# Kernel tuning notes

Hardware: AMD Instinct MI355X
Metric: run time of the kernel (lower is better)

## Reference

```python
import jax, jax.numpy as jnp
import numpy as np

N = 100000      # nodes
E = 300000      # edges
D_IN = 32       # input feature dim
D_MEM = 256     # memory dim
D_HID = 256     # hidden dim
D_TIME = 32     # time encoding dim
HEADS = 4
C = D_HID // 4  # per-head channels (GATConv out_channels)
D_OUT = 2


def gru_cell(x, h, wih, whh, bih, bhh):
    # torch.nn.GRUCell semantics, gate order (r, z, n)
    gi = x @ wih.T + bih
    gh = h @ whh.T + bhh
    ir, iz, inn = jnp.split(gi, 3, axis=-1)
    hr, hz, hn = jnp.split(gh, 3, axis=-1)
    r = jax.nn.sigmoid(ir + hr)
    z = jax.nn.sigmoid(iz + hz)
    n = jnp.tanh(inn + r * hn)
    return (1.0 - z) * n + z * h


def gat_layer(h, src, dst, W, a_src, a_dst, bias):
    # PyG GATConv(concat=True), default add_self_loops=True, negative_slope=0.2
    n = h.shape[0]
    xh = (h @ W.T).reshape(n, HEADS, C)              # [N,H,C]
    al_s = (xh * a_src).sum(-1)                      # [N,H]
    al_d = (xh * a_dst).sum(-1)                      # [N,H]
    loop = jnp.arange(n, dtype=src.dtype)
    s = jnp.concatenate([src, loop])
    d = jnp.concatenate([dst, loop])
    e = jax.nn.leaky_relu(al_s[s] + al_d[d], 0.2)    # [E+N,H]
    emax = jax.ops.segment_max(e, d, num_segments=n)
    ee = jnp.exp(e - emax[d])
    denom = jax.ops.segment_sum(ee, d, num_segments=n)
    alpha = ee / denom[d]                            # softmax over incoming edges
    out = jax.ops.segment_sum(alpha[:, :, None] * xh[s], d, num_segments=n)
    return out.reshape(n, HEADS * C) + bias


def setup_inputs() -> dict:
    key = jax.random.key(0)
    ks = jax.random.split(key, 32)
    w = lambda k, sh: jax.random.normal(k, sh, jnp.float32) * 0.05
    d_msg_in = 2 * D_MEM + D_IN + D_TIME  # 576
    return {
        "x": jax.random.normal(ks[0], (N, D_IN), jnp.float32),
        "timestamps": jax.random.uniform(ks[1], (E,), jnp.float32),
        "node_memory": jnp.zeros((N, D_MEM), jnp.float32),
        "last_update_time": jnp.zeros((N,), jnp.float32),
        "msg_w1": w(ks[2], (D_HID, d_msg_in)), "msg_b1": w(ks[3], (D_HID,)),
        "msg_w2": w(ks[4], (D_MEM, D_HID)), "msg_b2": w(ks[5], (D_MEM,)),
        "time_w1": w(ks[6], (D_TIME, 1)), "time_b1": w(ks[7], (D_TIME,)),
        "time_w2": w(ks[8], (D_TIME, D_TIME)), "time_b2": w(ks[9], (D_TIME,)),
        "gru_wih": w(ks[10], (3 * D_MEM, D_MEM)), "gru_whh": w(ks[11], (3 * D_MEM, D_MEM)),
        "gru_bih": w(ks[12], (3 * D_MEM,)), "gru_bhh": w(ks[13], (3 * D_MEM,)),
        "gat1_w": w(ks[14], (HEADS * C, D_MEM)), "gat1_asrc": w(ks[15], (HEADS, C)),
        "gat1_adst": w(ks[16], (HEADS, C)), "gat1_b": w(ks[17], (HEADS * C,)),
        "gat2_w": w(ks[18], (HEADS * C, D_HID)), "gat2_asrc": w(ks[19], (HEADS, C)),
        "gat2_adst": w(ks[20], (HEADS, C)), "gat2_b": w(ks[21], (HEADS * C,)),
        "cls_w1": w(ks[22], (D_HID // 2, D_HID)), "cls_b1": w(ks[23], (D_HID // 2,)),
        "cls_w2": w(ks[24], (D_OUT, D_HID // 2)), "cls_b2": w(ks[25], (D_OUT,)),
        "edge_index": jax.random.randint(ks[26], (2, E), 0, N, jnp.int32),
        "batch": jnp.zeros((N,), jnp.int32),
    }


def reference(x, timestamps, node_memory, last_update_time,
              msg_w1, msg_b1, msg_w2, msg_b2,
              time_w1, time_b1, time_w2, time_b2,
              gru_wih, gru_whh, gru_bih, gru_bhh,
              gat1_w, gat1_asrc, gat1_adst, gat1_b,
              gat2_w, gat2_asrc, gat2_adst, gat2_b,
              cls_w1, cls_b1, cls_w2, cls_b2,
              edge_index, batch):
    src, dst = edge_index[0], edge_index[1]
    edge_attr = x[src]                               # torch path: edge_attr=None -> x[edge_index[0]]
    current_time = timestamps.max()
    # --- compute_messages ---
    dt = (current_time - jnp.maximum(last_update_time[src], last_update_time[dst]))[:, None]
    te = jax.nn.relu(dt @ time_w1.T + time_b1) @ time_w2.T + time_b2
    mi = jnp.concatenate([node_memory[src], node_memory[dst], edge_attr, te], axis=-1)  # [E,576]
    msgs = jax.nn.relu(mi @ msg_w1.T + msg_b1) @ msg_w2.T + msg_b2                      # [E,256]
    # --- update_memory: fused segment-mean + batched GRU ---
    counts = jax.ops.segment_sum(jnp.ones((E,), msgs.dtype), dst, num_segments=N)
    agg = jax.ops.segment_sum(msgs, dst, num_segments=N) / jnp.maximum(counts, 1.0)[:, None]
    mem_new = gru_cell(agg, node_memory, gru_wih, gru_whh, gru_bih, gru_bhh)
    mem = jnp.where((counts > 0)[:, None], mem_new, node_memory)
    # --- GAT embedding layers (dropout inactive in eval) ---
    h = jax.nn.elu(gat_layer(mem, src, dst, gat1_w, gat1_asrc, gat1_adst, gat1_b))
    h = jax.nn.elu(gat_layer(h, src, dst, gat2_w, gat2_asrc, gat2_adst, gat2_b))
    # --- global mean pool (single graph, batch==0) + classifier ---
    gsum = jax.ops.segment_sum(h, batch, num_segments=1)
    gcnt = jax.ops.segment_sum(jnp.ones((N,), h.dtype), batch, num_segments=1)
    g = gsum / gcnt[:, None]
    logits = jax.nn.relu(g @ cls_w1.T + cls_b1) @ cls_w2.T + cls_b2
    return logits
```

## Files before the change

kernel.cpp:

```cpp
#include <hip/hip_runtime.h>

#define NN 100000
#define NE 300000
#define GPLANE 528

typedef float f32x4 __attribute__((ext_vector_type(4)));
typedef __bf16 bf16x8 __attribute__((ext_vector_type(8)));
typedef unsigned short ushort8v __attribute__((ext_vector_type(8)));

__device__ __forceinline__ int enc_f(float f) {
    int i = __float_as_int(f);
    return i >= 0 ? i : (i ^ 0x7fffffff);
}
__device__ __forceinline__ float dec_f(int i) {
    return __int_as_float(i >= 0 ? i : (i ^ 0x7fffffff));
}
__device__ __forceinline__ unsigned short f2bf(float f) {
    unsigned u = __float_as_uint(f);
    u += 0x7fffu + ((u >> 16) & 1u);
    return (unsigned short)(u >> 16);
}
__device__ __forceinline__ float bf2f(unsigned short u) {
    return __uint_as_float((unsigned)u << 16);
}

__global__ void k_dbg(float* out, float v) { out[0] = v; out[1] = v; }

__global__ void k_fill_i32(int* p, int v, int n) {
    int i = blockIdx.x * 256 + threadIdx.x;
    if (i < n) p[i] = v;
}

__global__ void k_pack_w_sub(const float* __restrict__ src, unsigned short* __restrict__ dst,
                             int OUT, int K, int stride, int off) {
    int i = blockIdx.x * 256 + threadIdx.x;
    if (i >= OUT * K) return;
    int o = i / K, k = i % K;
    int ob = o >> 6, n = (o >> 4) & 3, fr = o & 15;
    int step = k >> 5, kq = (k >> 3) & 3, j = k & 7;
    size_t dsti = ((((size_t)step * (OUT >> 6) + ob) * 4 + n) * 64 + (kq * 16 + fr)) * 8 + j;
    dst[dsti] = f2bf(src[(size_t)o * stride + off + k]);
}

__global__ void k_fold_te(const float* __restrict__ msg_w1, const float* __restrict__ tw2,
                          const float* __restrict__ tb2, const float* __restrict__ b1,
                          float* __restrict__ Mtd, float* __restrict__ b1eff) {
    int i = blockIdx.x * 256 + threadIdx.x;
    if (i < 256 * 32) {
        int o = i >> 5, col = i & 31;
        float s = 0.f;
        const float* w1d = msg_w1 + (size_t)o * 576 + 544;
#pragma unroll
        for (int c = 0; c < 32; ++c) s += w1d[c] * tw2[c * 32 + col];
        Mtd[i] = s;
        if (col == 0) {
            float sb = b1[o];
#pragma unroll
            for (int c = 0; c < 32; ++c) sb += w1d[c] * tb2[c];
            b1eff[o] = sb;
        }
    }
}

__global__ void k_timemax(const float* __restrict__ ts, int n, int* out) {
    float m = -INFINITY;
    int stride = gridDim.x * blockDim.x;
    for (int i = blockIdx.x * blockDim.x + threadIdx.x; i < n; i += stride)
        m = fmaxf(m, ts[i]);
    atomicMax(out, enc_f(m));
}

__global__ void k_counts(const int* __restrict__ ei, float* __restrict__ counts) {
    int stride = gridDim.x * blockDim.x;
    for (int i = blockIdx.x * blockDim.x + threadIdx.x; i < NE; i += stride)
        atomicAdd(&counts[ei[NE + i]], 1.f);
}

__global__ void k_scan1(const float* __restrict__ counts, int* __restrict__ rowptr,
                        int* __restrict__ bsum) {
    __shared__ int sh[256];
    int t = threadIdx.x;
    int i = blockIdx.x * 256 + t;
    int v = (i < NN) ? ((int)counts[i] + 1) : 0;
    sh[t] = v;
    __syncthreads();
    for (int off = 1; off < 256; off <<= 1) {
        int x = (t >= off) ? sh[t - off] : 0;
        __syncthreads();
        sh[t] += x;
        __syncthreads();
    }
    if (i < NN) rowptr[i + 1] = sh[t];
    if (t == 255) bsum[blockIdx.x] = sh[255];
}

__global__ void k_scan2(int* __restrict__ bsum, int nb) {
    __shared__ int sh[512];
    int t = threadIdx.x;
    sh[t] = (t < nb) ? bsum[t] : 0;
    __syncthreads();
    for (int off = 1; off < 512; off <<= 1) {
        int x = (t >= off) ? sh[t - off] : 0;
        __syncthreads();
        sh[t] += x;
        __syncthreads();
    }
    if (t < nb) bsum[t] = sh[t];
}

__global__ void k_scan3(int* __restrict__ rowptr, const int* __restrict__ bsum) {
    int i = blockIdx.x * 256 + threadIdx.x;
    if (i == 0) rowptr[0] = 0;
    if (i < NN) {
        int b = i >> 8;
        int off = b > 0 ? bsum[b - 1] : 0;
        rowptr[i + 1] += off;
    }
}

__global__ void k_copy_fill(const int* __restrict__ rowptr, int* __restrict__ fill) {
    int i = blockIdx.x * 256 + threadIdx.x;
    if (i < NN) fill[i] = rowptr[i];
}

__global__ void k_csr_fill(const int* __restrict__ ei, int* __restrict__ fill,
                           int* __restrict__ colidx) {
    int i = blockIdx.x * 256 + threadIdx.x;
    if (i < NE) {
        int d = ei[NE + i];
        int pos = atomicAdd(&fill[d], 1);
        colidx[pos] = ei[i];
    } else if (i < NE + NN) {
        int n = i - NE;
        int pos = atomicAdd(&fill[n], 1);
        colidx[pos] = n;
    }
}

__global__ void k_rowptrE(const int* __restrict__ rowptr, int* __restrict__ fillE) {
    int i = blockIdx.x * 256 + threadIdx.x;
    if (i < NN) fillE[i] = rowptr[i] - i;
}

__global__ void k_ecsr_fill(const int* __restrict__ ei, int* __restrict__ fillE,
                            int* __restrict__ esrc, int* __restrict__ edst) {
    int i = blockIdx.x * 256 + threadIdx.x;
    if (i < NE) {
        int d = ei[NE + i];
        int pos = atomicAdd(&fillE[d], 1);
        esrc[pos] = ei[i];
        edst[pos] = d;
    }
}

__global__ __launch_bounds__(512, 4) void k_pre1(
    const float* __restrict__ mem, const float* __restrict__ x,
    const unsigned short* __restrict__ w1ap, const unsigned short* __restrict__ w1bp,
    const unsigned short* __restrict__ w1cp,
    unsigned short* __restrict__ P13, unsigned short* __restrict__ P2,
    unsigned short* __restrict__ membf) {
    __shared__ unsigned short Af[2 * 8 * GPLANE];
    __shared__ unsigned short Axf[2 * 512];
    const int t = threadIdx.x;
    const int lane = t & 63, w = t >> 6;
    const int row0 = blockIdx.x * 32;
    const int frow = lane & 15, hi = lane >> 4;
    const int half = w >> 2, cq = w & 3;

    {
        int sr = t >> 4, sq = t & 15;
        int row = row0 + sr;
        const float* pm = mem + (size_t)row * 256 + sq * 16;
        int smq = sr >> 4, sfr = sr & 15;
#pragma unroll
        for (int j2 = 0; j2 < 2; ++j2) {
            int k8 = sq * 16 + j2 * 8;
            int st = k8 >> 5, kq = (k8 >> 3) & 3;
            float4 m0 = *(const float4*)(pm + j2 * 8);
            float4 m1 = *(const float4*)(pm + j2 * 8 + 4);
            ushort8v um;
            um[0] = f2bf(m0.x); um[1] = f2bf(m0.y); um[2] = f2bf(m0.z); um[3] = f2bf(m0.w);
            um[4] = f2bf(m1.x); um[5] = f2bf(m1.y); um[6] = f2bf(m1.z); um[7] = f2bf(m1.w);
            *(ushort8v*)&Af[((smq * 8) + st) * GPLANE + (kq * 16 + sfr) * 8] = um;
            *(ushort8v*)(membf + (size_t)row * 256 + k8) = um;
        }
    }
    if (t < 128) {
        int sr = t >> 2, sq = t & 3;
        int row = row0 + sr;
        const float* px = x + (size_t)row * 32 + sq * 8;
        float4 v0 = *(const float4*)px, v1 = *(const float4*)(px + 4);
        ushort8v u;
        u[0] = f2bf(v0.x); u[1] = f2bf(v0.y); u[2] = f2bf(v0.z); u[3] = f2bf(v0.w);
        u[4] = f2bf(v1.x); u[5] = f2bf(v1.y); u[6] = f2bf(v1.z); u[7] = f2bf(v1.w);
        *(ushort8v*)&Axf[(sr >> 4) * 512 + (sq * 16 + (sr & 15)) * 8] = u;
    }
    __syncthreads();

    f32x4 acc[2][4];
#pragma unroll
    for (int mf = 0; mf < 2; ++mf)
#pragma unroll
        for (int c = 0; c < 4; ++c) acc[mf][c] = (f32x4){0, 0, 0, 0};

    const unsigned short* wp = half ? w1bp : w1ap;
    for (int step = 0; step < 8; ++step) {
        bf16x8 aA[2];
#pragma unroll
        for (int mf = 0; mf < 2; ++mf)
            aA[mf] = *(const bf16x8*)&Af[((mf * 8) + step) * GPLANE + lane * 8];
#pragma unroll
        for (int ctl = 0; ctl < 4; ++ctl) {
            bf16x8 b = *(const bf16x8*)(wp + (((size_t)step * 4 + cq) * 4 + ctl) * 512 + lane * 8);
#pragma unroll
            for (int mf = 0; mf < 2; ++mf)
                acc[mf][ctl] = __builtin_amdgcn_mfma_f32_16x16x32_bf16(aA[mf], b, acc[mf][ctl], 0, 0, 0);
        }
    }
    if (half == 0) {
        bf16x8 aX[2];
#pragma unroll
        for (int mf = 0; mf < 2; ++mf)
            aX[mf] = *(const bf16x8*)&Axf[mf * 512 + lane * 8];
#pragma unroll
        for (int ctl = 0; ctl < 4; ++ctl) {
            bf16x8 b = *(const bf16x8*)(w1cp + (((size_t)0 * 4 + cq) * 4 + ctl) * 512 + lane * 8);
#pragma unroll
            for (int mf = 0; mf < 2; ++mf)
                acc[mf][ctl] = __builtin_amdgcn_mfma_f32_16x16x32_bf16(aX[mf], b, acc[mf][ctl], 0, 0, 0);
        }
    }
    unsigned short* P = half ? P2 : P13;
#pragma unroll
    for (int mf = 0; mf < 2; ++mf)
#pragma unroll
        for (int ctl = 0; ctl < 4; ++ctl) {
            int col = cq * 64 + ctl * 16 + frow;
#pragma unroll
            for (int r = 0; r < 4; ++r) {
                int row = row0 + mf * 16 + hi * 4 + r;
                P[(size_t)row * 256 + col] = f2bf(acc[mf][ctl][r]);
            }
        }
}

__global__ __launch_bounds__(256, 4) void k_msg_mfma(
    const int* __restrict__ ct, const float* __restrict__ lut,
    const int* __restrict__ esrc, const int* __restrict__ edst,
    const unsigned short* __restrict__ P13, const unsigned short* __restrict__ P2,
    const unsigned short* __restrict__ wtdp, const float* __restrict__ b1eff,
    const unsigned short* __restrict__ w2p, const float* __restrict__ b2,
    const float* __restrict__ tw1, const float* __restrict__ tb1,
    float* __restrict__ agg) {
    __shared__ unsigned short As[64][40];
    __shared__ unsigned short Hs[64][264];
    __shared__ int Da[64];

    const int t = threadIdx.x;
    const int lane = t & 63, wave = t >> 6;
    const int row0 = blockIdx.x * 64;
    const int frow = lane & 15;
    const int fk = (lane >> 4) * 8;
    const int hi = lane >> 4;
    const int col0w = wave * 64;

    if (t < 64) {
        int e = row0 + t;
        Da[t] = (e < NE) ? edst[e] : -1;
    }

    const int srow = t >> 2;
    const int skc = (t & 3) * 8;
    const int eIdx = row0 + srow;
    const bool ev = eIdx < NE;
    const int s_e = ev ? esrc[eIdx] : 0;
    const int d_e = ev ? edst[eIdx] : 0;

    {
        float ctv = dec_f(*ct);
        float dt = ev ? (ctv - fmaxf(lut[s_e], lut[d_e])) : 0.f;
        ushort8v u;
#pragma unroll
        for (int j = 0; j < 8; j++)
            u[j] = f2bf(fmaxf(dt * tw1[skc + j] + tb1[skc + j], 0.f));
        *(ushort8v*)&As[srow][skc] = u;
    }
#pragma unroll
    for (int q = 0; q < 8; ++q) {
        int c = skc + q * 32;
        ushort4 a0 = *(const ushort4*)(P13 + (size_t)s_e * 256 + c);
        ushort4 a1 = *(const ushort4*)(P13 + (size_t)s_e * 256 + c + 4);
        ushort4 b0 = *(const ushort4*)(P2 + (size_t)d_e * 256 + c);
        ushort4 b1v = *(const ushort4*)(P2 + (size_t)d_e * 256 + c + 4);
        ushort8v u;
        u[0] = f2bf(bf2f(a0.x) + bf2f(b0.x)); u[1] = f2bf(bf2f(a0.y) + bf2f(b0.y));
        u[2] = f2bf(bf2f(a0.z) + bf2f(b0.z)); u[3] = f2bf(bf2f(a0.w) + bf2f(b0.w));
        u[4] = f2bf(bf2f(a1.x) + bf2f(b1v.x)); u[5] = f2bf(bf2f(a1.y) + bf2f(b1v.y));
        u[6] = f2bf(bf2f(a1.z) + bf2f(b1v.z)); u[7] = f2bf(bf2f(a1.w) + bf2f(b1v.w));
        *(ushort8v*)&Hs[srow][c] = u;
    }
    __syncthreads();

    f32x4 acc[4][4];
#pragma unroll
    for (int m = 0; m < 4; m++)
#pragma unroll
        for (int n = 0; n < 4; n++) acc[m][n] = (f32x4){0.f, 0.f, 0.f, 0.f};

    {
        bf16x8 a[4];
#pragma unroll
        for (int m = 0; m < 4; m++)
            a[m] = *(const bf16x8*)&As[m * 16 + frow][fk];
#pragma unroll
        for (int n = 0; n < 4; n++) {
            bf16x8 b = *(const bf16x8*)(wtdp + (((size_t)0 * 4 + wave) * 4 + n) * 512 + lane * 8);
#pragma unroll
            for (int m = 0; m < 4; m++)
                acc[m][n] = __builtin_amdgcn_mfma_f32_16x16x32_bf16(a[m], b, acc[m][n], 0, 0, 0);
        }
    }
#pragma unroll
    for (int n = 0; n < 4; n++) {
        int c = col0w + n * 16 + frow;
        float bb = b1eff[c];
#pragma unroll
        for (int m = 0; m < 4; m++) {
#pragma unroll
            for (int r = 0; r < 4; r++) {
                int rr = m * 16 + hi * 4 + r;
                float v = acc[m][n][r] + bf2f(Hs[rr][c]) + bb;
                Hs[rr][c] = f2bf(fmaxf(v, 0.f));
            }
            acc[m][n] = (f32x4){0.f, 0.f, 0.f, 0.f};
        }
    }
    __syncthreads();

    bf16x8 bnext[4];
#pragma unroll
    for (int n = 0; n < 4; n++)
        bnext[n] = *(const bf16x8*)(w2p + (((size_t)0 * 4 + wave) * 4 + n) * 512 + lane * 8);
    for (int step = 0; step < 8; ++step) {
        const int k0 = step * 32;
        bf16x8 bcur[4];
#pragma unroll
        for (int n = 0; n < 4; n++) bcur[n] = bnext[n];
        if (step < 7) {
#pragma unroll
            for (int n = 0; n < 4; n++)
                bnext[n] = *(const bf16x8*)(w2p + (((size_t)(step + 1) * 4 + wave) * 4 + n) * 512 + lane * 8);
        }
        bf16x8 a[4];
#pragma unroll
        for (int m = 0; m < 4; m++)
            a[m] = *(const bf16x8*)&Hs[m * 16 + frow][k0 + fk];
#pragma unroll
        for (int m = 0; m < 4; m++)
#pragma unroll
            for (int n = 0; n < 4; n++)
                acc[m][n] = __builtin_amdgcn_mfma_f32_16x16x32_bf16(a[m], bcur[n], acc[m][n], 0, 0, 0);
    }

    __syncthreads();
    {
        float bb2[4];
#pragma unroll
        for (int n = 0; n < 4; n++) bb2[n] = b2[col0w + n * 16 + frow];
#pragma unroll
        for (int m = 0; m < 4; m++) {
            int rbase = m * 16 + hi * 4;
#pragma unroll
            for (int r = 0; r < 4; r++) {
#pragma unroll
                for (int n = 0; n < 4; n++)
                    Hs[rbase + r][col0w + n * 16 + frow] = f2bf(acc[m][n][r] + bb2[n]);
            }
        }
        __syncthreads();

        int nrows = min(64, NE - row0);
        float run = 0.f;
        int cur = Da[0];
        for (int i = 0; i < nrows; ++i) {
            int d = Da[i];
            if (d != cur) {
                atomicAdd(agg + (size_t)cur * 256 + t, run);
                run = 0.f;
                cur = d;
            }
            run += bf2f(Hs[i][t]);
        }
        atomicAdd(agg + (size_t)cur * 256 + t, run);
    }
}

__global__ __launch_bounds__(512, 4) void k_gru_mfma(
    const float* __restrict__ agg, const unsigned short* __restrict__ membf,
    const float* __restrict__ counts,
    const unsigned short* __restrict__ pwih, const unsigned short* __restrict__ pwhh,
    const float* __restrict__ bih, const float* __restrict__ bhh,
    unsigned short* __restrict__ memout) {
    __shared__ unsigned short Af[2 * 2 * 8 * GPLANE];
    const int t = threadIdx.x;
    const int lane = t & 63, w = t >> 6;
    const int row0 = blockIdx.x * 32;
    const int frow = lane & 15, hi = lane >> 4;
    const int cqp = blockIdx.y * 2 + (w >> 2);
    const int ctl = w & 3;

    {
        int sr = t >> 4, sq = t & 15;
        int row = row0 + sr;
        float inv = 1.f / fmaxf(counts[row], 1.f);
        const float* pa = agg + (size_t)row * 256 + sq * 16;
        const unsigned short* pm = membf + (size_t)row * 256 + sq * 16;
        int smq = sr >> 4, sfr = sr & 15;
#pragma unroll
        for (int j2 = 0; j2 < 2; ++j2) {
            int k8 = sq * 16 + j2 * 8;
            int st = k8 >> 5, kq = (k8 >> 3) & 3;
            float4 a0 = *(const float4*)(pa + j2 * 8);
            float4 a1 = *(const float4*)(pa + j2 * 8 + 4);
            ushort8v um = *(const ushort8v*)(pm + j2 * 8);
            ushort8v ua;
            ua[0] = f2bf(a0.x * inv); ua[1] = f2bf(a0.y * inv); ua[2] = f2bf(a0.z * inv); ua[3] = f2bf(a0.w * inv);
            ua[4] = f2bf(a1.x * inv); ua[5] = f2bf(a1.y * inv); ua[6] = f2bf(a1.z * inv); ua[7] = f2bf(a1.w * inv);
            int pos = kq * 16 + sfr;
            *(ushort8v*)&Af[(((0 * 2 + smq) * 8) + st) * GPLANE + pos * 8] = ua;
            *(ushort8v*)&Af[(((1 * 2 + smq) * 8) + st) * GPLANE + pos * 8] = um;
        }
    }
    __syncthreads();

    f32x4 rpre[2], zpre[2], inn[2], hn[2];
#pragma unroll
    for (int mf = 0; mf < 2; ++mf) {
        rpre[mf] = (f32x4){0, 0, 0, 0};
        zpre[mf] = (f32x4){0, 0, 0, 0};
        inn[mf]  = (f32x4){0, 0, 0, 0};
        hn[mf]   = (f32x4){0, 0, 0, 0};
    }

    for (int step = 0; step < 8; ++step) {
        bf16x8 aA[2], aM[2];
#pragma unroll
        for (int mf = 0; mf < 2; ++mf) {
            aA[mf] = *(const bf16x8*)&Af[(((0 * 2 + mf) * 8) + step) * GPLANE + lane * 8];
            aM[mf] = *(const bf16x8*)&Af[(((1 * 2 + mf) * 8) + step) * GPLANE + lane * 8];
        }
        size_t o_r = (((size_t)step * 12 + 0 * 4 + cqp) * 4 + ctl) * 512 + lane * 8;
        size_t o_z = (((size_t)step * 12 + 1 * 4 + cqp) * 4 + ctl) * 512 + lane * 8;
        size_t o_n = (((size_t)step * 12 + 2 * 4 + cqp) * 4 + ctl) * 512 + lane * 8;
        bf16x8 bIr = *(const bf16x8*)(pwih + o_r);
        bf16x8 bHr = *(const bf16x8*)(pwhh + o_r);
        bf16x8 bIz = *(const bf16x8*)(pwih + o_z);
        bf16x8 bHz = *(const bf16x8*)(pwhh + o_z);
        bf16x8 bIn = *(const bf16x8*)(pwih + o_n);
        bf16x8 bHn = *(const bf16x8*)(pwhh + o_n);
#pragma unroll
        for (int mf = 0; mf < 2; ++mf) {
            rpre[mf] = __builtin_amdgcn_mfma_f32_16x16x32_bf16(aA[mf], bIr, rpre[mf], 0, 0, 0);
            rpre[mf] = __builtin_amdgcn_mfma_f32_16x16x32_bf16(aM[mf], bHr, rpre[mf], 0, 0, 0);
            zpre[mf] = __builtin_amdgcn_mfma_f32_16x16x32_bf16(aA[mf], bIz, zpre[mf], 0, 0, 0);
            zpre[mf] = __builtin_amdgcn_mfma_f32_16x16x32_bf16(aM[mf], bHz, zpre[mf], 0, 0, 0);
            inn[mf]  = __builtin_amdgcn_mfma_f32_16x16x32_bf16(aA[mf], bIn, inn[mf], 0, 0, 0);
            hn[mf]   = __builtin_amdgcn_mfma_f32_16x16x32_bf16(aM[mf], bHn, hn[mf], 0, 0, 0);
        }
    }

    const int col = cqp * 64 + ctl * 16 + frow;
    const float br = bih[col] + bhh[col];
    const float bz = bih[256 + col] + bhh[256 + col];
    const float bin = bih[512 + col];
    const float bhn = bhh[512 + col];
#pragma unroll
    for (int mf = 0; mf < 2; ++mf)
#pragma unroll
        for (int r = 0; r < 4; ++r) {
            int row = row0 + mf * 16 + hi * 4 + r;
            float cnt = counts[row];
            float rg = 1.f / (1.f + expf(-(rpre[mf][r] + br)));
            float zg = 1.f / (1.f + expf(-(zpre[mf][r] + bz)));
            float ng = tanhf(inn[mf][r] + bin + rg * (hn[mf][r] + bhn));
            int pos = ((col >> 3) & 3) * 16 + (hi * 4 + r);
            float hp = bf2f(Af[(((1 * 2 + mf) * 8) + (col >> 5)) * GPLANE + pos * 8 + (col & 7)]);
            memout[(size_t)row * 256 + col] = f2bf((cnt > 0.f) ? ((1.f - zg) * ng + zg * hp) : hp);
        }
}

__global__ __launch_bounds__(256, 4) void k_xh_mfma(
    const unsigned short* __restrict__ A, const unsigned short* __restrict__ wp,
    const float* __restrict__ asrc, const float* __restrict__ adst,
    unsigned short* __restrict__ xh, float* __restrict__ als, float* __restrict__ ald) {
    const int t = threadIdx.x;
    const int lane = t & 63, w = t >> 6;
    const int row0 = blockIdx.x * 64;
    const int frow = lane & 15, fk = (lane >> 4) * 8, hi = lane >> 4;

    f32x4 acc[4][4];
#pragma unroll
    for (int m = 0; m < 4; m++)
#pragma unroll
        for (int c = 0; c < 4; c++) acc[m][c] = (f32x4){0, 0, 0, 0};

    for (int step = 0; step < 8; ++step) {
        const int k0 = step * 32;
        bf16x8 a[4];
#pragma unroll
        for (int m = 0; m < 4; ++m) {
            int row = min(row0 + m * 16 + frow, NN - 1);
            a[m] = *(const bf16x8*)(A + (size_t)row * 256 + k0 + fk);
        }
#pragma unroll
        for (int ctl = 0; ctl < 4; ++ctl) {
            bf16x8 b = *(const bf16x8*)(wp + (((size_t)step * 4 + w) * 4 + ctl) * 512 + lane * 8);
#pragma unroll
            for (int m = 0; m < 4; ++m)
                acc[m][ctl] = __builtin_amdgcn_mfma_f32_16x16x32_bf16(a[m], b, acc[m][ctl], 0, 0, 0);
        }
    }

    float asv[4], adv[4];
#pragma unroll
    for (int ctl = 0; ctl < 4; ++ctl) {
        asv[ctl] = asrc[w * 64 + ctl * 16 + frow];
        adv[ctl] = adst[w * 64 + ctl * 16 + frow];
    }
#pragma unroll
    for (int m = 0; m < 4; ++m) {
        float ps[4] = {0, 0, 0, 0}, pd[4] = {0, 0, 0, 0};
#pragma unroll
        for (int ctl = 0; ctl < 4; ++ctl) {
            int col = w * 64 + ctl * 16 + frow;
#pragma unroll
            for (int r = 0; r < 4; ++r) {
                float v = acc[m][ctl][r];
                ps[r] += v * asv[ctl];
                pd[r] += v * adv[ctl];
                int row = row0 + m * 16 + hi * 4 + r;
                if (row < NN) xh[(size_t)row * 256 + col] = f2bf(v);
            }
        }
#pragma unroll
        for (int off = 1; off < 16; off <<= 1) {
#pragma unroll
            for (int r = 0; r < 4; ++r) {
                ps[r] += __shfl_xor(ps[r], off, 64);
                pd[r] += __shfl_xor(pd[r], off, 64);
            }
        }
        if (frow == 0) {
#pragma unroll
            for (int r = 0; r < 4; ++r) {
                int row = row0 + m * 16 + hi * 4 + r;
                if (row < NN) { als[row * 4 + w] = ps[r]; ald[row * 4 + w] = pd[r]; }
            }
        }
    }
}

__global__ __launch_bounds__(256) void k_gat_csr(
    const int* __restrict__ rowptr, const int* __restrict__ colidx,
    const float* __restrict__ als, const float* __restrict__ ald,
    const unsigned short* __restrict__ xh, const float* __restrict__ bias,
    unsigned short* __restrict__ outb) {
    int d = blockIdx.x * 4 + (threadIdx.x >> 6);
    if (d >= NN) return;
    int lane = threadIdx.x & 63;
    int h = lane >> 4;
    int beg = rowptr[d], end = rowptr[d + 1];
    float aldv = ald[d * 4 + h];

    float m = -INFINITY;
    for (int p = beg; p < end; ++p) {
        int s = colidx[p];
        float e = als[s * 4 + h] + aldv;
        e = e > 0.f ? e : 0.2f * e;
        m = fmaxf(m, e);
    }
    float den = 0.f;
    float a0 = 0.f, a1 = 0.f, a2 = 0.f, a3 = 0.f;
    for (int p = beg; p < end; ++p) {
        int s = colidx[p];
        float e = als[s * 4 + h] + aldv;
        e = e > 0.f ? e : 0.2f * e;
        float pw = expf(e - m);
        den += pw;
        ushort4 uv = *(const ushort4*)(xh + (size_t)s * 256 + lane * 4);
        a0 += pw * bf2f(uv.x);
        a1 += pw * bf2f(uv.y);
        a2 += pw * bf2f(uv.z);
        a3 += pw * bf2f(uv.w);
    }
    float inv = 1.f / den;
    int c = lane * 4;
    float4 bv = *(const float4*)(bias + c);
    float ox = a0 * inv + bv.x; ox = ox > 0.f ? ox : expm1f(ox);
    float oy = a1 * inv + bv.y; oy = oy > 0.f ? oy : expm1f(oy);
    float oz = a2 * inv + bv.z; oz = oz > 0.f ? oz : expm1f(oz);
    float ow = a3 * inv + bv.w; ow = ow > 0.f ? ow : expm1f(ow);
    ushort4 o;
    o.x = f2bf(ox); o.y = f2bf(oy); o.z = f2bf(oz); o.w = f2bf(ow);
    *(ushort4*)(outb + (size_t)d * 256 + c) = o;
}

__global__ __launch_bounds__(256) void k_pool(const unsigned short* __restrict__ h,
                                              const int* __restrict__ batch, float* __restrict__ gsum) {
    int t = threadIdx.x;
    const int per = (NN + gridDim.x - 1) / gridDim.x;
    int n0 = blockIdx.x * per, n1 = min(NN, n0 + per);
    float s = 0.f, cnt = 0.f;
    for (int n = n0; n < n1; n++) {
        if (batch[n] == 0) {
            s += bf2f(h[(size_t)n * 256 + t]);
            cnt += 1.f;
        }
    }
    atomicAdd(&gsum[t], s);
    if (t == 0) atomicAdd(&gsum[256], cnt);
}

__global__ void k_cls(const float* __restrict__ gsum, const float* __restrict__ w1,
                      const float* __restrict__ b1, const float* __restrict__ w2,
                      const float* __restrict__ b2, float* __restrict__ out) {
    __shared__ float g[256];
    __shared__ float hid[128];
    int t = threadIdx.x;
    float gc = gsum[256];
    g[t] = gsum[t] / gc;
    __syncthreads();
    if (t < 128) {
        float s = b1[t];
        for (int k = 0; k < 256; k++) s += g[k] * w1[t * 256 + k];
        hid[t] = fmaxf(s, 0.f);
    }
    __syncthreads();
    if (t < 2) {
        float s = b2[t];
        for (int k = 0; k < 128; k++) s += hid[k] * w2[t * 128 + k];
        out[t] = s;
    }
}

extern "C" void kernel_launch(void* const* d_in, const int* in_sizes, int n_in,
                              void* d_out, int out_size, void* d_ws, size_t ws_size,
                              hipStream_t stream) {
    const float* xv      = (const float*)d_in[0];
    const float* tsv     = (const float*)d_in[1];
    const float* nodemem = (const float*)d_in[2];
    const float* lut     = (const float*)d_in[3];
    const float* msg_w1  = (const float*)d_in[4];
    const float* msg_b1  = (const float*)d_in[5];
    const float* msg_w2  = (const float*)d_in[6];
    const float* msg_b2  = (const float*)d_in[7];
    const float* time_w1 = (const float*)d_in[8];
    const float* time_b1 = (const float*)d_in[9];
    const float* time_w2 = (const float*)d_in[10];
    const float* time_b2 = (const float*)d_in[11];
    const float* gru_wih = (const float*)d_in[12];
    const float* gru_whh = (const float*)d_in[13];
    const float* gru_bih = (const float*)d_in[14];
    const float* gru_bhh = (const float*)d_in[15];
    const float* gat1_w    = (const float*)d_in[16];
    const float* gat1_asrc = (const float*)d_in[17];
    const float* gat1_adst = (const float*)d_in[18];
    const float* gat1_b    = (const float*)d_in[19];
    const float* gat2_w    = (const float*)d_in[20];
    const float* gat2_asrc = (const float*)d_in[21];
    const float* gat2_adst = (const float*)d_in[22];
    const float* gat2_b    = (const float*)d_in[23];
    const float* cls_w1 = (const float*)d_in[24];
    const float* cls_b1 = (const float*)d_in[25];
    const float* cls_w2 = (const float*)d_in[26];
    const float* cls_b2 = (const float*)d_in[27];
    const int* ei    = (const int*)d_in[28];
    const int* batch = (const int*)d_in[29];
    float* out = (float*)d_out;

    char* wsb = (char*)d_ws;
    size_t off = 0;
    auto carve = [&](size_t bytes) {
        char* p = wsb + off;
        off += (bytes + 255) & ~(size_t)255;
        return p;
    };
    int*   curtime = (int*)carve(4);
    unsigned short* w1ap = (unsigned short*)carve((size_t)256 * 256 * 2);
    unsigned short* w1bp = (unsigned short*)carve((size_t)256 * 256 * 2);
    unsigned short* w1cp = (unsigned short*)carve((size_t)256 * 32 * 2);
    unsigned short* wtdp = (unsigned short*)carve((size_t)256 * 32 * 2);
    unsigned short* w2p  = (unsigned short*)carve((size_t)256 * 256 * 2);
    unsigned short* wihp = (unsigned short*)carve((size_t)768 * 256 * 2);
    unsigned short* whhp = (unsigned short*)carve((size_t)768 * 256 * 2);
    unsigned short* g1p  = (unsigned short*)carve((size_t)256 * 256 * 2);
    unsigned short* g2p  = (unsigned short*)carve((size_t)256 * 256 * 2);
    float* Mtd   = (float*)carve((size_t)256 * 32 * 4);
    float* b1eff = (float*)carve(256 * 4);
    unsigned short* P13  = (unsigned short*)carve((size_t)NN * 256 * 2);
    unsigned short* P2   = (unsigned short*)carve((size_t)NN * 256 * 2);
    unsigned short* membf = (unsigned short*)carve((size_t)NN * 256 * 2);
    float* als    = (float*)carve((size_t)NN * 4 * 4);
    float* ald    = (float*)carve((size_t)NN * 4 * 4);
    float* counts = (float*)carve((size_t)NN * 4);
    float* gsum   = (float*)carve(257 * 4);
    int*   rowptr = (int*)carve((size_t)(NN + 1) * 4);
    int*   colidx = (int*)carve((size_t)(NE + NN) * 4);
    int*   fillp  = (int*)carve((size_t)NN * 4);
    int*   bsum   = (int*)carve(512 * 4);
    int*   esrc   = (int*)carve((size_t)NE * 4);
    int*   edst   = (int*)carve((size_t)NE * 4);
    int*   fillE  = (int*)carve((size_t)NN * 4);
    float* R1     = (float*)carve((size_t)NN * 256 * 4);
    float* R2     = (float*)carve((size_t)NN * 256 * 4);

    if (ws_size < off) {
        k_dbg<<<1, 1, 0, stream>>>(out, (float)(ws_size >> 20));
        return;
    }

    float* agg   = R1;
    unsigned short* memo  = (unsigned short*)R2;
    unsigned short* xh1   = (unsigned short*)R1;
    unsigned short* xh2   = (unsigned short*)R1;
    unsigned short* outb1 = (unsigned short*)R2;
    unsigned short* outb2 = (unsigned short*)R2;

    hipMemsetAsync(agg, 0, (size_t)NN * 256 * 4, stream);
    hipMemsetAsync(counts, 0, (size_t)NN * 4, stream);
    hipMemsetAsync(gsum, 0, 257 * 4, stream);
    k_fill_i32<<<1, 256, 0, stream>>>(curtime, (int)0x80000000, 1);

    k_fold_te<<<32, 256, 0, stream>>>(msg_w1, time_w2, time_b2, msg_b1, Mtd, b1eff);
    k_pack_w_sub<<<256, 256, 0, stream>>>(msg_w1, w1ap, 256, 256, 576, 0);
    k_pack_w_sub<<<256, 256, 0, stream>>>(msg_w1, w1bp, 256, 256, 576, 256);
    k_pack_w_sub<<<32, 256, 0, stream>>>(msg_w1, w1cp, 256, 32, 576, 512);
    k_pack_w_sub<<<32, 256, 0, stream>>>(Mtd, wtdp, 256, 32, 32, 0);
    k_pack_w_sub<<<256, 256, 0, stream>>>(msg_w2, w2p, 256, 256, 256, 0);
    k_pack_w_sub<<<768, 256, 0, stream>>>(gru_wih, wihp, 768, 256, 256, 0);
    k_pack_w_sub<<<768, 256, 0, stream>>>(gru_whh, whhp, 768, 256, 256, 0);
    k_pack_w_sub<<<256, 256, 0, stream>>>(gat1_w, g1p, 256, 256, 256, 0);
    k_pack_w_sub<<<256, 256, 0, stream>>>(gat2_w, g2p, 256, 256, 256, 0);

    k_counts<<<1024, 256, 0, stream>>>(ei, counts);
    k_scan1<<<391, 256, 0, stream>>>(counts, rowptr, bsum);
    k_scan2<<<1, 512, 0, stream>>>(bsum, 391);
    k_scan3<<<391, 256, 0, stream>>>(rowptr, bsum);
    k_copy_fill<<<391, 256, 0, stream>>>(rowptr, fillp);
    k_csr_fill<<<1563, 256, 0, stream>>>(ei, fillp, colidx);
    k_rowptrE<<<391, 256, 0, stream>>>(rowptr, fillE);
    k_ecsr_fill<<<1172, 256, 0, stream>>>(ei, fillE, esrc, edst);

    k_timemax<<<512, 256, 0, stream>>>(tsv, NE, curtime);
    k_pre1<<<3125, 512, 0, stream>>>(nodemem, xv, w1ap, w1bp, w1cp, P13, P2, membf);
    k_msg_mfma<<<4688, 256, 0, stream>>>(curtime, lut, esrc, edst, P13, P2,
                                         wtdp, b1eff, w2p, msg_b2,
                                         time_w1, time_b1, agg);
    k_gru_mfma<<<dim3(3125, 2), 512, 0, stream>>>(agg, membf, counts, wihp, whhp,
                                                  gru_bih, gru_bhh, memo);

    k_xh_mfma<<<1563, 256, 0, stream>>>(memo, g1p, gat1_asrc, gat1_adst, xh1, als, ald);
    k_gat_csr<<<25000, 256, 0, stream>>>(rowptr, colidx, als, ald, xh1, gat1_b, outb1);

    k_xh_mfma<<<1563, 256, 0, stream>>>(outb1, g2p, gat2_asrc, gat2_adst, xh2, als, ald);
    k_gat_csr<<<25000, 256, 0, stream>>>(rowptr, colidx, als, ald, xh2, gat2_b, outb2);

    k_pool<<<2048, 256, 0, stream>>>(outb2, batch, gsum);
    k_cls<<<1, 256, 0, stream>>>(gsum, cls_w1, cls_b1, cls_w2, cls_b2, out);
}
```

Before: 830.9 us.

## Widen message kernel to eight waves and fold fill-array init into scan

The message MLP kernel now runs 512 threads per block instead of 256. Each of the eight waves computes 32 output columns instead of 64, and the final segment reduction is split between two row halves. This aims to raise the number of waves per CU and shorten per-thread work, at the cost of less weight-fragment reuse and possibly more atomics at the row-half boundary. Separately, the copy_fill and rowptrE kernels are merged into the scan3 kernel, which removes two launches and one extra pass over rowptr.

```diff
diff --git a/kernel.cpp b/kernel.cpp
--- a/kernel.cpp
+++ b/kernel.cpp
@@ -108,19 +108,24 @@
     if (t < nb) bsum[t] = sh[t];
 }
 
-__global__ void k_scan3(int* __restrict__ rowptr, const int* __restrict__ bsum) {
+__global__ void k_scan3(int* __restrict__ rowptr, const int* __restrict__ bsum,
+                        int* __restrict__ fillp, int* __restrict__ fillE) {
     int i = blockIdx.x * 256 + threadIdx.x;
-    if (i == 0) rowptr[0] = 0;
+    if (i == 0) {
+        rowptr[0] = 0;
+        fillp[0] = 0;
+        fillE[0] = 0;
+    }
     if (i < NN) {
         int b = i >> 8;
         int off = b > 0 ? bsum[b - 1] : 0;
-        rowptr[i + 1] += off;
-    }
-}
-
-__global__ void k_copy_fill(const int* __restrict__ rowptr, int* __restrict__ fill) {
-    int i = blockIdx.x * 256 + threadIdx.x;
-    if (i < NN) fill[i] = rowptr[i];
+        int v = rowptr[i + 1] + off;
+        rowptr[i + 1] = v;
+        if (i + 1 < NN) {
+            fillp[i + 1] = v;
+            fillE[i + 1] = v - (i + 1);
+        }
+    }
 }
 
 __global__ void k_csr_fill(const int* __restrict__ ei, int* __restrict__ fill,
@@ -135,11 +140,6 @@
         int pos = atomicAdd(&fill[n], 1);
         colidx[pos] = n;
     }
-}
-
-__global__ void k_rowptrE(const int* __restrict__ rowptr, int* __restrict__ fillE) {
-    int i = blockIdx.x * 256 + threadIdx.x;
-    if (i < NN) fillE[i] = rowptr[i] - i;
 }
 
 __global__ void k_ecsr_fill(const int* __restrict__ ei, int* __restrict__ fillE,
@@ -244,7 +244,7 @@
         }
 }
 
-__global__ __launch_bounds__(256, 4) void k_msg_mfma(
+__global__ __launch_bounds__(512, 4) void k_msg_mfma(
     const int* __restrict__ ct, const float* __restrict__ lut,
     const int* __restrict__ esrc, const int* __restrict__ edst,
     const unsigned short* __restrict__ P13, const unsigned short* __restrict__ P2,
@@ -262,15 +262,16 @@
     const int frow = lane & 15;
     const int fk = (lane >> 4) * 8;
     const int hi = lane >> 4;
-    const int col0w = wave * 64;
+    const int wb = wave >> 1;
+    const int wn = (wave & 1) * 2;
 
     if (t < 64) {
         int e = row0 + t;
         Da[t] = (e < NE) ? edst[e] : -1;
     }
 
-    const int srow = t >> 2;
-    const int skc = (t & 3) * 8;
+    const int srow = t >> 3;
+    const int sj = t & 7;
     const int eIdx = row0 + srow;
     const bool ev = eIdx < NE;
     const int s_e = ev ? esrc[eIdx] : 0;
@@ -279,15 +280,17 @@
     {
         float ctv = dec_f(*ct);
         float dt = ev ? (ctv - fmaxf(lut[s_e], lut[d_e])) : 0.f;
-        ushort8v u;
-#pragma unroll
-        for (int j = 0; j < 8; j++)
-            u[j] = f2bf(fmaxf(dt * tw1[skc + j] + tb1[skc + j], 0.f));
-        *(ushort8v*)&As[srow][skc] = u;
-    }
-#pragma unroll
-    for (int q = 0; q < 8; ++q) {
-        int c = skc + q * 32;
+        ushort4 u;
+        int c0 = sj * 4;
+        u.x = f2bf(fmaxf(dt * tw1[c0 + 0] + tb1[c0 + 0], 0.f));
+        u.y = f2bf(fmaxf(dt * tw1[c0 + 1] + tb1[c0 + 1], 0.f));
+        u.z = f2bf(fmaxf(dt * tw1[c0 + 2] + tb1[c0 + 2], 0.f));
+        u.w = f2bf(fmaxf(dt * tw1[c0 + 3] + tb1[c0 + 3], 0.f));
+        *(ushort4*)&As[srow][c0] = u;
+    }
+#pragma unroll
+    for (int q = 0; q < 4; ++q) {
+        int c = sj * 8 + q * 64;
         ushort4 a0 = *(const ushort4*)(P13 + (size_t)s_e * 256 + c);
         ushort4 a1 = *(const ushort4*)(P13 + (size_t)s_e * 256 + c + 4);
         ushort4 b0 = *(const ushort4*)(P2 + (size_t)d_e * 256 + c);
@@ -301,11 +304,11 @@
     }
     __syncthreads();
 
-    f32x4 acc[4][4];
+    f32x4 acc[4][2];
 #pragma unroll
     for (int m = 0; m < 4; m++)
 #pragma unroll
-        for (int n = 0; n < 4; n++) acc[m][n] = (f32x4){0.f, 0.f, 0.f, 0.f};
+        for (int n = 0; n < 2; n++) acc[m][n] = (f32x4){0.f, 0.f, 0.f, 0.f};
 
     {
         bf16x8 a[4];
@@ -313,16 +316,16 @@
         for (int m = 0; m < 4; m++)
             a[m] = *(const bf16x8*)&As[m * 16 + frow][fk];
 #pragma unroll
-        for (int n = 0; n < 4; n++) {
-            bf16x8 b = *(const bf16x8*)(wtdp + (((size_t)0 * 4 + wave) * 4 + n) * 512 + lane * 8);
+        for (int n = 0; n < 2; n++) {
+            bf16x8 b = *(const bf16x8*)(wtdp + (((size_t)0 * 4 + wb) * 4 + (wn + n)) * 512 + lane * 8);
 #pragma unroll
             for (int m = 0; m < 4; m++)
                 acc[m][n] = __builtin_amdgcn_mfma_f32_16x16x32_bf16(a[m], b, acc[m][n], 0, 0, 0);
         }
     }
 #pragma unroll
-    for (int n = 0; n < 4; n++) {
-        int c = col0w + n * 16 + frow;
+    for (int n = 0; n < 2; n++) {
+        int c = wave * 32 + n * 16 + frow;
         float bb = b1eff[c];
 #pragma unroll
         for (int m = 0; m < 4; m++) {
@@ -337,19 +340,19 @@
     }
     __syncthreads();
 
-    bf16x8 bnext[4];
-#pragma unroll
-    for (int n = 0; n < 4; n++)
-        bnext[n] = *(const bf16x8*)(w2p + (((size_t)0 * 4 + wave) * 4 + n) * 512 + lane * 8);
+    bf16x8 bnext[2];
+#pragma unroll
+    for (int n = 0; n < 2; n++)
+        bnext[n] = *(const bf16x8*)(w2p + (((size_t)0 * 4 + wb) * 4 + (wn + n)) * 512 + lane * 8);
     for (int step = 0; step < 8; ++step) {
         const int k0 = step * 32;
-        bf16x8 bcur[4];
-#pragma unroll
-        for (int n = 0; n < 4; n++) bcur[n] = bnext[n];
+        bf16x8 bcur[2];
+#pragma unroll
+        for (int n = 0; n < 2; n++) bcur[n] = bnext[n];
         if (step < 7) {
 #pragma unroll
-            for (int n = 0; n < 4; n++)
-                bnext[n] = *(const bf16x8*)(w2p + (((size_t)(step + 1) * 4 + wave) * 4 + n) * 512 + lane * 8);
+            for (int n = 0; n < 2; n++)
+                bnext[n] = *(const bf16x8*)(w2p + (((size_t)(step + 1) * 4 + wb) * 4 + (wn + n)) * 512 + lane * 8);
         }
         bf16x8 a[4];
 #pragma unroll
@@ -358,40 +361,45 @@
 #pragma unroll
         for (int m = 0; m < 4; m++)
 #pragma unroll
-            for (int n = 0; n < 4; n++)
+            for (int n = 0; n < 2; n++)
                 acc[m][n] = __builtin_amdgcn_mfma_f32_16x16x32_bf16(a[m], bcur[n], acc[m][n], 0, 0, 0);
     }
 
     __syncthreads();
     {
-        float bb2[4];
-#pragma unroll
-        for (int n = 0; n < 4; n++) bb2[n] = b2[col0w + n * 16 + frow];
+        float bb2[2];
+#pragma unroll
+        for (int n = 0; n < 2; n++) bb2[n] = b2[wave * 32 + n * 16 + frow];
 #pragma unroll
         for (int m = 0; m < 4; m++) {
             int rbase = m * 16 + hi * 4;
 #pragma unroll
             for (int r = 0; r < 4; r++) {
 #pragma unroll
-                for (int n = 0; n < 4; n++)
-                    Hs[rbase + r][col0w + n * 16 + frow] = f2bf(acc[m][n][r] + bb2[n]);
+                for (int n = 0; n < 2; n++)
+                    Hs[rbase + r][wave * 32 + n * 16 + frow] = f2bf(acc[m][n][r] + bb2[n]);
             }
         }
         __syncthreads();
 
         int nrows = min(64, NE - row0);
-        float run = 0.f;
-        int cur = Da[0];
-        for (int i = 0; i < nrows; ++i) {
-            int d = Da[i];
-            if (d != cur) {
-                atomicAdd(agg + (size_t)cur * 256 + t, run);
-                run = 0.f;
-                cur = d;
+        int col = t & 255;
+        int rs = (t >> 8) * 32;
+        int re = min(nrows, rs + 32);
+        if (rs < re) {
+            float run = 0.f;
+            int cur = Da[rs];
+            for (int i = rs; i < re; ++i) {
+                int d = Da[i];
+                if (d != cur) {
+                    atomicAdd(agg + (size_t)cur * 256 + col, run);
+                    run = 0.f;
+                    cur = d;
+                }
+                run += bf2f(Hs[i][col]);
             }
-            run += bf2f(Hs[i][t]);
-        }
-        atomicAdd(agg + (size_t)cur * 256 + t, run);
+            atomicAdd(agg + (size_t)cur * 256 + col, run);
+        }
     }
 }
 
@@ -745,15 +753,13 @@
     k_counts<<<1024, 256, 0, stream>>>(ei, counts);
     k_scan1<<<391, 256, 0, stream>>>(counts, rowptr, bsum);
     k_scan2<<<1, 512, 0, stream>>>(bsum, 391);
-    k_scan3<<<391, 256, 0, stream>>>(rowptr, bsum);
-    k_copy_fill<<<391, 256, 0, stream>>>(rowptr, fillp);
+    k_scan3<<<391, 256, 0, stream>>>(rowptr, bsum, fillp, fillE);
     k_csr_fill<<<1563, 256, 0, stream>>>(ei, fillp, colidx);
-    k_rowptrE<<<391, 256, 0, stream>>>(rowptr, fillE);
     k_ecsr_fill<<<1172, 256, 0, stream>>>(ei, fillE, esrc, edst);
 
     k_timemax<<<512, 256, 0, stream>>>(tsv, NE, curtime);
     k_pre1<<<3125, 512, 0, stream>>>(nodemem, xv, w1ap, w1bp, w1cp, P13, P2, membf);
-    k_msg_mfma<<<4688, 256, 0, stream>>>(curtime, lut, esrc, edst, P13, P2,
+    k_msg_mfma<<<4688, 512, 0, stream>>>(curtime, lut, esrc, edst, P13, P2,
                                          wtdp, b1eff, w2p, msg_b2,
                                          time_w1, time_b1, agg);
     k_gru_mfma<<<dim3(3125, 2), 512, 0, stream>>>(agg, membf, counts, wihp, whhp,
```

After: 810.2 us (median of 2 runs). 1.03x faster.
